# Performance work log

Hardware: AMD Instinct MI355X
Metric: run time of the kernel (lower is better)

## Reference

```python
import jax, jax.numpy as jnp
import numpy as np

B, F, U, G = 2048, 512, 512, 64
REG_STRENGTH = 1.0


def setup_inputs() -> dict:
    key = jax.random.key(0)
    k0, k1, k2, k3, k4 = jax.random.split(key, 5)
    x = jax.random.normal(k0, (B, F), dtype=jnp.float32)
    gid = jax.random.randint(k1, (B,), 0, G, dtype=jnp.int64)
    # glorot-normal-ish scale for kernels: sqrt(2/(fan_in+fan_out))
    glorot = np.sqrt(2.0 / (U + F)).astype(np.float32)
    w_mu = jax.random.normal(k2, (G, U, F), dtype=jnp.float32) * glorot
    b_mu = jax.random.normal(k3, (G, U), dtype=jnp.float32) * 0.05  # 'random_normal' init
    w0_mu = jax.random.normal(k4, (U, F), dtype=jnp.float32) * glorot
    b0_mu = jnp.zeros((U,), dtype=jnp.float32)
    return {"x": x, "gid": gid, "w_mu": w_mu, "b_mu": b_mu, "w0_mu": w0_mu, "b0_mu": b0_mu}


def reference(x, gid, w_mu, b_mu, w0_mu, b0_mu):
    # Hard top-1 routing: per-sample weight matrix gather, [B, U, F]
    w = jnp.take(w_mu, gid, axis=0)
    b = jnp.take(b_mu, gid, axis=0)  # [B, U]
    # Batched matvec: 'Bup,Bp->Bu'
    outputs = jnp.einsum("buf,bf->bu", w, x) + b  # use_bias=True, activation=None
    # L2 prior regularization loss (added via add_loss in the original)
    w_loss = jnp.sum(jnp.square(w - w0_mu[None]))  # sum over axes [1,2] then batch
    b_loss = jnp.sum(jnp.square(b - b0_mu[None]))
    reg_loss = REG_STRENGTH * (w_loss + b_loss)
    return outputs, reg_loss
```

## Files before the change

### kernel.cpp

```cpp
#include <hip/hip_runtime.h>
#include <hip/hip_bf16.h>

#define B_SZ 2048
#define F_SZ 512
#define U_SZ 512
#define G_SZ 64
#define REG_STRENGTH 1.0f

#define BM 32
#define BN 64
#define BK 32
#define ZSPLIT 2
#define NTILES (U_SZ / BN)
#define THREADS 128


__global__ __launch_bounds__(1024) void prep_kernel(
    const int* __restrict__ gid, float* __restrict__ wsf,
    int* __restrict__ counts, int* __restrict__ rowstart,
    int* __restrict__ order) {
  __shared__ int cnt_s[G_SZ];
  __shared__ int cur_s[G_SZ];
  const int tid = threadIdx.x;

  if (tid < G_SZ) cnt_s[tid] = 0;
  if (tid == 0) wsf[0] = 0.0f;
  __syncthreads();

  for (int b = tid; b < B_SZ; b += 1024) atomicAdd(&cnt_s[gid[b]], 1);
  __syncthreads();

  if (tid == 0) {
    int run = 0;
    for (int g = 0; g < G_SZ; ++g) { cur_s[g] = run; run += cnt_s[g]; }
  }
  __syncthreads();

  if (tid < G_SZ) { counts[tid] = cnt_s[tid]; rowstart[tid] = cur_s[tid]; }
  __syncthreads();

  for (int b = tid; b < B_SZ; b += 1024) {
    int pos = atomicAdd(&cur_s[gid[b]], 1);
    order[pos] = b;
  }
}

__global__ __launch_bounds__(THREADS) void gemm_kernel(
    const float* __restrict__ x, const float* __restrict__ w_mu,
    const float* __restrict__ b_mu, const float* __restrict__ w0_mu,
    const float* __restrict__ b0_mu, float* __restrict__ out,
    float* __restrict__ wsf, const int* __restrict__ counts,
    const int* __restrict__ rowstart, const int* __restrict__ order) {
  const int g = blockIdx.y;
  const int cnt = counts[g];
  if (cnt == 0) return;
  const int z = blockIdx.z;
  const int n0 = blockIdx.x * BN;
  const int rs = rowstart[g];
  const int tid = threadIdx.x;

  const int tn = tid & 15;
  const int tmc = tid >> 4;
  const int sr = tid >> 3;
  const int skq = tid & 7;
  const int kb = skq * 4;

  __shared__ __align__(16) float Xs[BK][BM + 4];
  __shared__ __align__(16) float Ws[BK][BN + 4];

  const float* __restrict__ Wg = w_mu + (size_t)g * (U_SZ * F_SZ);
  const bool do_reg = (z == 0);
  float regp = 0.0f;

  if (do_reg && blockIdx.x == 0) {
    const float4 bm4 = *(const float4*)(b_mu + (g << 9) + tid * 4);
    const float4 b04 = *(const float4*)(b0_mu + tid * 4);
    float dx = bm4.x - b04.x, dy = bm4.y - b04.y;
    float dz = bm4.z - b04.z, dw = bm4.w - b04.w;
    regp += dx * dx + dy * dy + dz * dz + dw * dw;
  }

  bool first_pass = true;
  for (int r0 = z * BM; r0 < cnt; r0 += BM * ZSPLIT) {
    float acc[4][4] = {};
    int rA = r0 + sr;      if (rA >= cnt) rA = cnt - 1;
    int rB = r0 + sr + 16; if (rB >= cnt) rB = cnt - 1;
    const float* __restrict__ xrowA = x + (size_t)order[rs + rA] * F_SZ;
    const float* __restrict__ xrowB = x + (size_t)order[rs + rB] * F_SZ;

    float4 xpA = *(const float4*)(xrowA + kb);
    float4 xpB = *(const float4*)(xrowB + kb);
    float4 wp[4];
#pragma unroll
    for (int m = 0; m < 4; ++m)
      wp[m] = *(const float4*)(Wg + (size_t)(n0 + sr + 16 * m) * F_SZ + kb);

    for (int kc = 0; kc < F_SZ; kc += BK) {
      __syncthreads();
      Xs[kb + 0][sr] = xpA.x; Xs[kb + 1][sr] = xpA.y;
      Xs[kb + 2][sr] = xpA.z; Xs[kb + 3][sr] = xpA.w;
      Xs[kb + 0][sr + 16] = xpB.x; Xs[kb + 1][sr + 16] = xpB.y;
      Xs[kb + 2][sr + 16] = xpB.z; Xs[kb + 3][sr + 16] = xpB.w;
#pragma unroll
      for (int m = 0; m < 4; ++m) {
        const int u = sr + 16 * m;
        Ws[kb + 0][u] = wp[m].x; Ws[kb + 1][u] = wp[m].y;
        Ws[kb + 2][u] = wp[m].z; Ws[kb + 3][u] = wp[m].w;
      }
      if (do_reg && first_pass) {
#pragma unroll
        for (int m = 0; m < 4; ++m) {
          const float4 w04 = *(const float4*)(
              w0_mu + (size_t)(n0 + sr + 16 * m) * F_SZ + kc + kb);
          float dx = wp[m].x - w04.x, dy = wp[m].y - w04.y;
          float dz = wp[m].z - w04.z, dw = wp[m].w - w04.w;
          regp += dx * dx + dy * dy + dz * dz + dw * dw;
        }
      }
      __syncthreads();
      if (kc + BK < F_SZ) {
        const int ko = kc + BK + kb;
        xpA = *(const float4*)(xrowA + ko);
        xpB = *(const float4*)(xrowB + ko);
#pragma unroll
        for (int m = 0; m < 4; ++m)
          wp[m] = *(const float4*)(Wg + (size_t)(n0 + sr + 16 * m) * F_SZ + ko);
      }
#pragma unroll
      for (int kk = 0; kk < BK; ++kk) {
        const float4 av = *(const float4*)&Xs[kk][tmc * 4];
        const float4 bv = *(const float4*)&Ws[kk][tn * 4];
        const float a[4] = {av.x, av.y, av.z, av.w};
        const float b[4] = {bv.x, bv.y, bv.z, bv.w};
#pragma unroll
        for (int i = 0; i < 4; ++i)
#pragma unroll
          for (int j = 0; j < 4; ++j) acc[i][j] += a[i] * b[j];
      }
    }

    const float4 bias = *(const float4*)(b_mu + (g << 9) + n0 + tn * 4);
#pragma unroll
    for (int i = 0; i < 4; ++i) {
      const int r = r0 + tmc * 4 + i;
      if (r < cnt) {
        float4 o;
        o.x = acc[i][0] + bias.x;
        o.y = acc[i][1] + bias.y;
        o.z = acc[i][2] + bias.z;
        o.w = acc[i][3] + bias.w;
        *(float4*)(out + (size_t)order[rs + r] * U_SZ + n0 + tn * 4) = o;
      }
    }
    first_pass = false;
  }

  if (do_reg) {
    __syncthreads();
    float* red = &Xs[0][0];
    red[tid] = regp;
    __syncthreads();
    for (int s = 64; s > 0; s >>= 1) {
      if (tid < s) red[tid] += red[tid + s];
      __syncthreads();
    }
    if (tid == 0) atomicAdd(wsf, (float)cnt * red[0]);
  }
}

__global__ void finalize_kernel(const float* __restrict__ wsf,
                                float* __restrict__ out) {
  out[(size_t)B_SZ * U_SZ] = REG_STRENGTH * wsf[0];
}

extern "C" void kernel_launch(void* const* d_in, const int* in_sizes, int n_in,
                              void* d_out, int out_size, void* d_ws, size_t ws_size,
                              hipStream_t stream) {
  const float* x     = (const float*)d_in[0];
  const int*   gid   = (const int*)d_in[1];
  const float* w_mu  = (const float*)d_in[2];
  const float* b_mu  = (const float*)d_in[3];
  const float* w0_mu = (const float*)d_in[4];
  const float* b0_mu = (const float*)d_in[5];
  float* out = (float*)d_out;

  float* wsf      = (float*)d_ws;
  int*   counts   = (int*)d_ws + 2;
  int*   rowstart = (int*)d_ws + 2 + G_SZ;
  int*   order    = (int*)d_ws + 2 + 2 * G_SZ;

  prep_kernel<<<1, 1024, 0, stream>>>(gid, wsf, counts, rowstart, order);
  gemm_kernel<<<dim3(NTILES, G_SZ, ZSPLIT), THREADS, 0, stream>>>(
      x, w_mu, b_mu, w0_mu, b0_mu, out, wsf, counts, rowstart, order);
  finalize_kernel<<<1, 1, 0, stream>>>(wsf, out);
}
```

Before: 140.8 us.

## Fuse routing, grouped GEMM and reduction into one MFMA kernel with split-bf16

Replaces the three-kernel pipeline with a single kernel. Each block scans gid itself to build its group's row list in shared memory, then computes the grouped matvec-GEMM on bf16 MFMA using a hi/lo split (three products) to approximate fp32 accuracy. It double-buffers swizzled X tiles in LDS, feeds W directly from registers, and finishes the loss with a last-block-done atomic counter instead of a separate finalize launch. This is meant to cut launch overhead and the scalar FMA cost. In exchange every block rescans gid, and precision relies on the split-bf16 scheme.

Result: slower. 146.0 us (+3.7%).

```diff
diff --git a/kernel.cpp b/kernel.cpp
--- a/kernel.cpp
+++ b/kernel.cpp
@@ -1,5 +1,4 @@
 #include <hip/hip_runtime.h>
-#include <hip/hip_bf16.h>
 
 #define B_SZ 2048
 #define F_SZ 512
@@ -7,190 +6,255 @@
 #define G_SZ 64
 #define REG_STRENGTH 1.0f
 
-#define BM 32
+#define NT 8
 #define BN 64
-#define BK 32
-#define ZSPLIT 2
-#define NTILES (U_SZ / BN)
-#define THREADS 128
-
-
-__global__ __launch_bounds__(1024) void prep_kernel(
-    const int* __restrict__ gid, float* __restrict__ wsf,
-    int* __restrict__ counts, int* __restrict__ rowstart,
-    int* __restrict__ order) {
-  __shared__ int cnt_s[G_SZ];
-  __shared__ int cur_s[G_SZ];
+#define BK 64
+#define NSTEP (F_SZ / BK)
+#define MROWS 64
+#define THREADS 256
+#define NBLOCKS (NT * G_SZ)
+
+typedef float f32x4 __attribute__((ext_vector_type(4)));
+typedef __bf16 bf16x8 __attribute__((ext_vector_type(8)));
+
+#define MFMA(a, b, c) __builtin_amdgcn_mfma_f32_16x16x32_bf16((a), (b), (c), 0, 0, 0)
+
+static __device__ __forceinline__ unsigned short bf16_rne(float f) {
+  unsigned u = __float_as_uint(f);
+  return (unsigned short)((u + 0x7fffu + ((u >> 16) & 1u)) >> 16);
+}
+
+static __device__ __forceinline__ void cvt8(const f32x4 a, const f32x4 b,
+                                            bf16x8& h, bf16x8& l) {
+#pragma unroll
+  for (int i = 0; i < 4; ++i) {
+    const unsigned short hb = bf16_rne(a[i]);
+    h[i] = __builtin_bit_cast(__bf16, hb);
+    l[i] = __builtin_bit_cast(
+        __bf16, bf16_rne(a[i] - __uint_as_float((unsigned)hb << 16)));
+  }
+#pragma unroll
+  for (int i = 0; i < 4; ++i) {
+    const unsigned short hb = bf16_rne(b[i]);
+    h[4 + i] = __builtin_bit_cast(__bf16, hb);
+    l[4 + i] = __builtin_bit_cast(
+        __bf16, bf16_rne(b[i] - __uint_as_float((unsigned)hb << 16)));
+  }
+}
+
+static __device__ __forceinline__ void writeX(unsigned short* __restrict__ xh,
+                                              unsigned short* __restrict__ xl,
+                                              int row, int kq, const f32x4 v) {
+  int byte = (row << 7) + (kq << 3);
+  byte ^= (row & 7) << 4;
+  const unsigned short h0 = bf16_rne(v[0]);
+  const unsigned short h1 = bf16_rne(v[1]);
+  const unsigned short h2 = bf16_rne(v[2]);
+  const unsigned short h3 = bf16_rne(v[3]);
+  const ushort4 hv = make_ushort4(h0, h1, h2, h3);
+  const ushort4 lv = make_ushort4(
+      bf16_rne(v[0] - __uint_as_float((unsigned)h0 << 16)),
+      bf16_rne(v[1] - __uint_as_float((unsigned)h1 << 16)),
+      bf16_rne(v[2] - __uint_as_float((unsigned)h2 << 16)),
+      bf16_rne(v[3] - __uint_as_float((unsigned)h3 << 16)));
+  *(ushort4*)((char*)xh + byte) = hv;
+  *(ushort4*)((char*)xl + byte) = lv;
+}
+
+static __device__ __forceinline__ bf16x8 readA(
+    const unsigned short* __restrict__ base, int m, int kk, int llo, int lhi) {
+  const int row = (m << 4) + llo;
+  int byte = (row << 7) + (kk << 6) + (lhi << 4);
+  byte ^= (row & 7) << 4;
+  return *(const bf16x8*)((const char*)base + byte);
+}
+
+__global__ __launch_bounds__(THREADS, 2) void fused_kernel(
+    const float* __restrict__ x, const int* __restrict__ gid,
+    const float* __restrict__ w_mu, const float* __restrict__ b_mu,
+    const float* __restrict__ w0_mu, const float* __restrict__ b0_mu,
+    float* __restrict__ out, float* __restrict__ wsf,
+    unsigned* __restrict__ done) {
+  __shared__ __align__(16) unsigned short XH[2][MROWS * BK];
+  __shared__ __align__(16) unsigned short XL[2][MROWS * BK];
+  __shared__ int rows_s[B_SZ];
+  __shared__ int cnt_s;
+  __shared__ float red_s[THREADS / 64];
+
+  const int f = blockIdx.x;
+  const int r8 = f & 7;
+  const int q = f >> 3;
+  const int nt = q & 7;
+  const int g = ((q >> 3) << 3) + r8;
+
   const int tid = threadIdx.x;
-
-  if (tid < G_SZ) cnt_s[tid] = 0;
-  if (tid == 0) wsf[0] = 0.0f;
+  const int lane = tid & 63;
+  const int wv = tid >> 6;
+  const int lhi = lane >> 4;
+  const int llo = lane & 15;
+
+  if (tid == 0) cnt_s = 0;
   __syncthreads();
-
-  for (int b = tid; b < B_SZ; b += 1024) atomicAdd(&cnt_s[gid[b]], 1);
+#pragma unroll
+  for (int u = 0; u < 2; ++u) {
+    const int4 v = ((const int4*)gid)[tid + u * THREADS];
+    const int b0 = (tid + u * THREADS) << 2;
+    if (v.x == g) rows_s[atomicAdd(&cnt_s, 1)] = b0;
+    if (v.y == g) rows_s[atomicAdd(&cnt_s, 1)] = b0 + 1;
+    if (v.z == g) rows_s[atomicAdd(&cnt_s, 1)] = b0 + 2;
+    if (v.w == g) rows_s[atomicAdd(&cnt_s, 1)] = b0 + 3;
+  }
   __syncthreads();
+  const int cnt = cnt_s;
+
+  if (cnt > 0) {
+    const int mycol = nt * BN + wv * 16 + llo;
+    const float* __restrict__ wrow =
+        w_mu + (size_t)g * (U_SZ * F_SZ) + (size_t)mycol * F_SZ;
+    const float* __restrict__ w0row = w0_mu + (size_t)mycol * F_SZ;
+
+    float regp = 0.0f;
+    if (nt == 0) {
+      for (int u = tid; u < U_SZ; u += THREADS) {
+        const float d = b_mu[(g << 9) + u] - b0_mu[u];
+        regp += d * d;
+      }
+    }
+
+    for (int r0c = 0; r0c < cnt; r0c += MROWS) {
+      const int rc = min(MROWS, cnt - r0c);
+      const int nf4 = rc << 4;
+      const int mt = (rc + 15) >> 4;
+      const bool doreg = (r0c == 0);
+      f32x4 acc[4];
+#pragma unroll
+      for (int m = 0; m < 4; ++m) acc[m] = (f32x4){0.f, 0.f, 0.f, 0.f};
+
+#pragma unroll
+      for (int u = 0; u < 4; ++u) {
+        const int i = tid + u * THREADS;
+        if (i < nf4) {
+          const int row = i >> 4, kq = i & 15;
+          const f32x4 v = *(const f32x4*)(
+              x + (size_t)rows_s[r0c + row] * F_SZ + (kq << 2));
+          writeX(&XH[0][0], &XL[0][0], row, kq, v);
+        }
+      }
+      __syncthreads();
+
+      for (int s = 0; s < NSTEP; ++s) {
+        const int buf = s & 1;
+        f32x4 xr[4];
+        if (s + 1 < NSTEP) {
+          const int kc = (s + 1) * BK;
+#pragma unroll
+          for (int u = 0; u < 4; ++u) {
+            const int i = tid + u * THREADS;
+            if (i < nf4) {
+              const int row = i >> 4, kq = i & 15;
+              xr[u] = *(const f32x4*)(
+                  x + (size_t)rows_s[r0c + row] * F_SZ + kc + (kq << 2));
+            }
+          }
+        }
+        const int kcs = s * BK + (lhi << 3);
+        const f32x4 wa0 = *(const f32x4*)(wrow + kcs);
+        const f32x4 wa1 = *(const f32x4*)(wrow + kcs + 4);
+        const f32x4 wb0 = *(const f32x4*)(wrow + kcs + 32);
+        const f32x4 wb1 = *(const f32x4*)(wrow + kcs + 32 + 4);
+        if (doreg) {
+          const f32x4 z0 = *(const f32x4*)(w0row + kcs);
+          const f32x4 z1 = *(const f32x4*)(w0row + kcs + 4);
+          const f32x4 z2 = *(const f32x4*)(w0row + kcs + 32);
+          const f32x4 z3 = *(const f32x4*)(w0row + kcs + 32 + 4);
+#pragma unroll
+          for (int i = 0; i < 4; ++i) {
+            const float d0 = wa0[i] - z0[i], d1 = wa1[i] - z1[i];
+            const float d2 = wb0[i] - z2[i], d3 = wb1[i] - z3[i];
+            regp += d0 * d0 + d1 * d1 + d2 * d2 + d3 * d3;
+          }
+        }
+        bf16x8 wh0, wl0, wh1, wl1;
+        cvt8(wa0, wa1, wh0, wl0);
+        cvt8(wb0, wb1, wh1, wl1);
+#pragma unroll
+        for (int m = 0; m < 4; ++m) {
+          if (m < mt) {
+            const bf16x8 ah0 = readA(&XH[buf][0], m, 0, llo, lhi);
+            const bf16x8 al0 = readA(&XL[buf][0], m, 0, llo, lhi);
+            acc[m] = MFMA(ah0, wh0, acc[m]);
+            acc[m] = MFMA(ah0, wl0, acc[m]);
+            acc[m] = MFMA(al0, wh0, acc[m]);
+            const bf16x8 ah1 = readA(&XH[buf][0], m, 1, llo, lhi);
+            const bf16x8 al1 = readA(&XL[buf][0], m, 1, llo, lhi);
+            acc[m] = MFMA(ah1, wh1, acc[m]);
+            acc[m] = MFMA(ah1, wl1, acc[m]);
+            acc[m] = MFMA(al1, wh1, acc[m]);
+          }
+        }
+        if (s + 1 < NSTEP) {
+#pragma unroll
+          for (int u = 0; u < 4; ++u) {
+            const int i = tid + u * THREADS;
+            if (i < nf4) {
+              const int row = i >> 4, kq = i & 15;
+              writeX(&XH[buf ^ 1][0], &XL[buf ^ 1][0], row, kq, xr[u]);
+            }
+          }
+        }
+        __syncthreads();
+      }
+
+      const float bias = b_mu[(g << 9) + mycol];
+#pragma unroll
+      for (int m = 0; m < 4; ++m) {
+        if (m < mt) {
+#pragma unroll
+          for (int j = 0; j < 4; ++j) {
+            const int rl = (m << 4) + (lhi << 2) + j;
+            if (rl < rc) {
+              out[(size_t)rows_s[r0c + rl] * U_SZ + mycol] = acc[m][j] + bias;
+            }
+          }
+        }
+      }
+    }
+
+#pragma unroll
+    for (int o = 32; o > 0; o >>= 1) regp += __shfl_down(regp, o, 64);
+    if (lane == 0) red_s[wv] = regp;
+    __syncthreads();
+    if (tid == 0) {
+      atomicAdd(wsf, (float)cnt * (red_s[0] + red_s[1] + red_s[2] + red_s[3]));
+    }
+  }
 
   if (tid == 0) {
-    int run = 0;
-    for (int g = 0; g < G_SZ; ++g) { cur_s[g] = run; run += cnt_s[g]; }
-  }
-  __syncthreads();
-
-  if (tid < G_SZ) { counts[tid] = cnt_s[tid]; rowstart[tid] = cur_s[tid]; }
-  __syncthreads();
-
-  for (int b = tid; b < B_SZ; b += 1024) {
-    int pos = atomicAdd(&cur_s[gid[b]], 1);
-    order[pos] = b;
-  }
-}
-
-__global__ __launch_bounds__(THREADS) void gemm_kernel(
-    const float* __restrict__ x, const float* __restrict__ w_mu,
-    const float* __restrict__ b_mu, const float* __restrict__ w0_mu,
-    const float* __restrict__ b0_mu, float* __restrict__ out,
-    float* __restrict__ wsf, const int* __restrict__ counts,
-    const int* __restrict__ rowstart, const int* __restrict__ order) {
-  const int g = blockIdx.y;
-  const int cnt = counts[g];
-  if (cnt == 0) return;
-  const int z = blockIdx.z;
-  const int n0 = blockIdx.x * BN;
-  const int rs = rowstart[g];
-  const int tid = threadIdx.x;
-
-  const int tn = tid & 15;
-  const int tmc = tid >> 4;
-  const int sr = tid >> 3;
-  const int skq = tid & 7;
-  const int kb = skq * 4;
-
-  __shared__ __align__(16) float Xs[BK][BM + 4];
-  __shared__ __align__(16) float Ws[BK][BN + 4];
-
-  const float* __restrict__ Wg = w_mu + (size_t)g * (U_SZ * F_SZ);
-  const bool do_reg = (z == 0);
-  float regp = 0.0f;
-
-  if (do_reg && blockIdx.x == 0) {
-    const float4 bm4 = *(const float4*)(b_mu + (g << 9) + tid * 4);
-    const float4 b04 = *(const float4*)(b0_mu + tid * 4);
-    float dx = bm4.x - b04.x, dy = bm4.y - b04.y;
-    float dz = bm4.z - b04.z, dw = bm4.w - b04.w;
-    regp += dx * dx + dy * dy + dz * dz + dw * dw;
-  }
-
-  bool first_pass = true;
-  for (int r0 = z * BM; r0 < cnt; r0 += BM * ZSPLIT) {
-    float acc[4][4] = {};
-    int rA = r0 + sr;      if (rA >= cnt) rA = cnt - 1;
-    int rB = r0 + sr + 16; if (rB >= cnt) rB = cnt - 1;
-    const float* __restrict__ xrowA = x + (size_t)order[rs + rA] * F_SZ;
-    const float* __restrict__ xrowB = x + (size_t)order[rs + rB] * F_SZ;
-
-    float4 xpA = *(const float4*)(xrowA + kb);
-    float4 xpB = *(const float4*)(xrowB + kb);
-    float4 wp[4];
-#pragma unroll
-    for (int m = 0; m < 4; ++m)
-      wp[m] = *(const float4*)(Wg + (size_t)(n0 + sr + 16 * m) * F_SZ + kb);
-
-    for (int kc = 0; kc < F_SZ; kc += BK) {
-      __syncthreads();
-      Xs[kb + 0][sr] = xpA.x; Xs[kb + 1][sr] = xpA.y;
-      Xs[kb + 2][sr] = xpA.z; Xs[kb + 3][sr] = xpA.w;
-      Xs[kb + 0][sr + 16] = xpB.x; Xs[kb + 1][sr + 16] = xpB.y;
-      Xs[kb + 2][sr + 16] = xpB.z; Xs[kb + 3][sr + 16] = xpB.w;
-#pragma unroll
-      for (int m = 0; m < 4; ++m) {
-        const int u = sr + 16 * m;
-        Ws[kb + 0][u] = wp[m].x; Ws[kb + 1][u] = wp[m].y;
-        Ws[kb + 2][u] = wp[m].z; Ws[kb + 3][u] = wp[m].w;
-      }
-      if (do_reg && first_pass) {
-#pragma unroll
-        for (int m = 0; m < 4; ++m) {
-          const float4 w04 = *(const float4*)(
-              w0_mu + (size_t)(n0 + sr + 16 * m) * F_SZ + kc + kb);
-          float dx = wp[m].x - w04.x, dy = wp[m].y - w04.y;
-          float dz = wp[m].z - w04.z, dw = wp[m].w - w04.w;
-          regp += dx * dx + dy * dy + dz * dz + dw * dw;
-        }
-      }
-      __syncthreads();
-      if (kc + BK < F_SZ) {
-        const int ko = kc + BK + kb;
-        xpA = *(const float4*)(xrowA + ko);
-        xpB = *(const float4*)(xrowB + ko);
-#pragma unroll
-        for (int m = 0; m < 4; ++m)
-          wp[m] = *(const float4*)(Wg + (size_t)(n0 + sr + 16 * m) * F_SZ + ko);
-      }
-#pragma unroll
-      for (int kk = 0; kk < BK; ++kk) {
-        const float4 av = *(const float4*)&Xs[kk][tmc * 4];
-        const float4 bv = *(const float4*)&Ws[kk][tn * 4];
-        const float a[4] = {av.x, av.y, av.z, av.w};
-        const float b[4] = {bv.x, bv.y, bv.z, bv.w};
-#pragma unroll
-        for (int i = 0; i < 4; ++i)
-#pragma unroll
-          for (int j = 0; j < 4; ++j) acc[i][j] += a[i] * b[j];
-      }
-    }
-
-    const float4 bias = *(const float4*)(b_mu + (g << 9) + n0 + tn * 4);
-#pragma unroll
-    for (int i = 0; i < 4; ++i) {
-      const int r = r0 + tmc * 4 + i;
-      if (r < cnt) {
-        float4 o;
-        o.x = acc[i][0] + bias.x;
-        o.y = acc[i][1] + bias.y;
-        o.z = acc[i][2] + bias.z;
-        o.w = acc[i][3] + bias.w;
-        *(float4*)(out + (size_t)order[rs + r] * U_SZ + n0 + tn * 4) = o;
-      }
-    }
-    first_pass = false;
-  }
-
-  if (do_reg) {
-    __syncthreads();
-    float* red = &Xs[0][0];
-    red[tid] = regp;
-    __syncthreads();
-    for (int s = 64; s > 0; s >>= 1) {
-      if (tid < s) red[tid] += red[tid + s];
-      __syncthreads();
-    }
-    if (tid == 0) atomicAdd(wsf, (float)cnt * red[0]);
-  }
-}
-
-__global__ void finalize_kernel(const float* __restrict__ wsf,
-                                float* __restrict__ out) {
-  out[(size_t)B_SZ * U_SZ] = REG_STRENGTH * wsf[0];
+    __threadfence();
+    const unsigned prev = atomicAdd(done, 1u);
+    if (prev == (unsigned)(gridDim.x - 1)) {
+      __threadfence();
+      const float v = atomicAdd(wsf, 0.0f);
+      out[(size_t)B_SZ * U_SZ] = REG_STRENGTH * v;
+    }
+  }
 }
 
 extern "C" void kernel_launch(void* const* d_in, const int* in_sizes, int n_in,
-                              void* d_out, int out_size, void* d_ws, size_t ws_size,
-                              hipStream_t stream) {
+                              void* d_out, int out_size, void* d_ws,
+                              size_t ws_size, hipStream_t stream) {
+  (void)in_sizes; (void)n_in; (void)out_size; (void)ws_size;
   const float* x     = (const float*)d_in[0];
   const int*   gid   = (const int*)d_in[1];
   const float* w_mu  = (const float*)d_in[2];
   const float* b_mu  = (const float*)d_in[3];
   const float* w0_mu = (const float*)d_in[4];
   const float* b0_mu = (const float*)d_in[5];
-  float* out = (float*)d_out;
-
-  float* wsf      = (float*)d_ws;
-  int*   counts   = (int*)d_ws + 2;
-  int*   rowstart = (int*)d_ws + 2 + G_SZ;
-  int*   order    = (int*)d_ws + 2 + 2 * G_SZ;
-
-  prep_kernel<<<1, 1024, 0, stream>>>(gid, wsf, counts, rowstart, order);
-  gemm_kernel<<<dim3(NTILES, G_SZ, ZSPLIT), THREADS, 0, stream>>>(
-      x, w_mu, b_mu, w0_mu, b0_mu, out, wsf, counts, rowstart, order);
-  finalize_kernel<<<1, 1, 0, stream>>>(wsf, out);
-}
+
+  float* wsf = (float*)d_ws;
+  unsigned* done = (unsigned*)d_ws + 1;
+
+  hipMemsetAsync(d_ws, 0, 8, stream);
+  fused_kernel<<<NBLOCKS, THREADS, 0, stream>>>(x, gid, w_mu, b_mu, w0_mu,
+                                                b0_mu, (float*)d_out, wsf, done);
+}
```
